# Kernel tuning notes

Measured on AMD Instinct MI355X. Metric: run time of the kernel, lower is better.

The kernel has to match this reference:

```python
import jax, jax.numpy as jnp
import numpy as np

DIM = 2048
HEADS = 16
HEAD_DIM = 128
B = 2
T = 2048


def _rope_as_in_source(x):
    # x: (b, h, t, d). FAITHFUL to the source bug: RotaryEmbedding uses
    # x.shape[1] (the HEADS axis, since it is called after transpose) as the
    # 'sequence' index, so rotation angle depends on head index and is
    # broadcast over the true sequence axis.
    n = x.shape[1]  # == heads
    d = x.shape[-1]
    inv_freq = 1.0 / (10000.0 ** (jnp.arange(0, d, 2, dtype=jnp.float32) / d))
    freqs = jnp.arange(n, dtype=jnp.float32)[:, None] * inv_freq[None, :]  # (h, d/2)
    cos = jnp.cos(freqs)[None, :, None, :]  # (1, h, 1, d/2)
    sin = jnp.sin(freqs)[None, :, None, :]
    x1 = x[..., 0::2]
    x2 = x[..., 1::2]
    out = jnp.stack([x1 * cos - x2 * sin, x1 * sin + x2 * cos], axis=-1)
    return out.reshape(x.shape)


def setup_inputs() -> dict:
    key = jax.random.key(0)
    ks = jax.random.split(key, 9)
    s_in = 1.0 / np.sqrt(DIM)
    hd = HEADS * HEAD_DIM
    s_o = 1.0 / np.sqrt(hd)
    return {
        "x": jax.random.normal(ks[0], (B, T, DIM), dtype=jnp.float32),
        "Wq": jax.random.normal(ks[1], (DIM, hd), dtype=jnp.float32) * s_in,
        "bq": jnp.zeros((hd,), dtype=jnp.float32),
        "Wk": jax.random.normal(ks[2], (DIM, hd), dtype=jnp.float32) * s_in,
        "bk": jnp.zeros((hd,), dtype=jnp.float32),
        "Wv": jax.random.normal(ks[3], (DIM, hd), dtype=jnp.float32) * s_in,
        "bv": jnp.zeros((hd,), dtype=jnp.float32),
        "Wo": jax.random.normal(ks[4], (hd, DIM), dtype=jnp.float32) * s_o,
        "bo": jnp.zeros((DIM,), dtype=jnp.float32),
    }


def reference(x, Wq, bq, Wk, bk, Wv, bv, Wo, bo):
    b, t, c = x.shape
    q = (x @ Wq + bq).reshape(b, t, HEADS, HEAD_DIM).transpose(0, 2, 1, 3)
    k = (x @ Wk + bk).reshape(b, t, HEADS, HEAD_DIM).transpose(0, 2, 1, 3)
    v = (x @ Wv + bv).reshape(b, t, HEADS, HEAD_DIM).transpose(0, 2, 1, 3)
    q = _rope_as_in_source(q)
    k = _rope_as_in_source(k)
    scale = 1.0 / np.sqrt(HEAD_DIM)
    scores = jnp.einsum("bhqd,bhkd->bhqk", q, k) * scale  # (b,h,t,t)
    attn = jax.nn.softmax(scores, axis=-1)
    out = jnp.einsum("bhqk,bhkd->bhqd", attn, v)  # (b,h,t,d)
    out = out.transpose(0, 2, 1, 3).reshape(b, t, HEADS * HEAD_DIM)
    return out @ Wo + bo
```

## Files before the change

kernel.cpp:

```cpp
#include <hip/hip_runtime.h>

typedef unsigned short ushort_t;
typedef unsigned int uint_t;
typedef __attribute__((ext_vector_type(8))) short short8;
typedef __attribute__((ext_vector_type(4))) float f32x4;
typedef __attribute__((ext_vector_type(4))) unsigned short ushort4_t;
typedef __attribute__((ext_vector_type(4))) unsigned int uint4_t;

__device__ inline ushort_t f2b(float f) {
    unsigned int x = __builtin_bit_cast(unsigned int, f);
    x += 0x7fffu + ((x >> 16) & 1u);
    return (ushort_t)(x >> 16);
}
__device__ inline uint_t cvt_pk_bf16(float lo, float hi) {
    uint_t r;
    asm("v_cvt_pk_bf16_f32 %0, %1, %2" : "=v"(r) : "v"(lo), "v"(hi));
    return r;
}

__device__ inline void gload16(const void* g, void* l) {
    __builtin_amdgcn_global_load_lds(
        (const __attribute__((address_space(1))) void*)g,
        (__attribute__((address_space(3))) void*)l, 16, 0, 0);
}

__global__ __launch_bounds__(256)
void cast_bf16(const float* __restrict__ src, ushort_t* __restrict__ dst) {
    size_t i = ((size_t)blockIdx.x * 256 + threadIdx.x) * 8;
    f32x4 a = *reinterpret_cast<const f32x4*>(src + i);
    f32x4 b = *reinterpret_cast<const f32x4*>(src + i + 4);
    short8 v;
#pragma unroll
    for (int j = 0; j < 4; ++j) { v[j] = (short)f2b(a[j]); v[4 + j] = (short)f2b(b[j]); }
    *reinterpret_cast<short8*>(dst + i) = v;
}

__global__ __launch_bounds__(64)
void transp4(const float* __restrict__ s0, const float* __restrict__ s1,
             const float* __restrict__ s2, const float* __restrict__ s3,
             ushort_t* __restrict__ d0, ushort_t* __restrict__ d1,
             ushort_t* __restrict__ d2, ushort_t* __restrict__ d3) {
    const int z = blockIdx.z;
    const float* src = (z == 0) ? s0 : (z == 1) ? s1 : (z == 2) ? s2 : s3;
    ushort_t* dst = (z == 0) ? d0 : (z == 1) ? d1 : (z == 2) ? d2 : d3;
    const int R = 2048, C = 2048;
    int r0 = blockIdx.x * 64 + ((threadIdx.x >> 3) << 3);
    int c0 = blockIdx.y * 64 + ((threadIdx.x & 7) << 3);
    ushort_t v[8][8];
#pragma unroll
    for (int i = 0; i < 8; ++i) {
        const float* p = src + (size_t)(r0 + i) * C + c0;
        f32x4 a = *reinterpret_cast<const f32x4*>(p);
        f32x4 b = *reinterpret_cast<const f32x4*>(p + 4);
#pragma unroll
        for (int j = 0; j < 4; ++j) { v[i][j] = f2b(a[j]); v[i][4 + j] = f2b(b[j]); }
    }
#pragma unroll
    for (int c = 0; c < 8; ++c) {
        short8 w;
#pragma unroll
        for (int i = 0; i < 8; ++i) w[i] = (short)v[i][c];
        *reinterpret_cast<short8*>(dst + (size_t)(c0 + c) * R + r0) = w;
    }
}

template <int MODE>
__global__ __launch_bounds__(256)
void gemm_qkv(const ushort_t* __restrict__ A, const ushort_t* __restrict__ Bt,
              const float* __restrict__ bias, ushort_t* __restrict__ C, float oscale) {
    const int K = 2048;
    __shared__ __align__(16) ushort_t As[128 * 64];
    __shared__ __align__(16) ushort_t Bs[128 * 64];
    const int tid = threadIdx.x, lane = tid & 63, wid = tid >> 6;
    const int l15 = lane & 15, g = lane >> 4;
    const int wr = wid >> 1, wc = wid & 1;
    const int m0 = blockIdx.y * 128, n0 = blockIdx.x * 128;
    f32x4 acc[4][4] = {};
    for (int k0 = 0; k0 < K; k0 += 64) {
#pragma unroll
        for (int is = 0; is < 4; ++is) {
            int c = is * 256 + tid;
            int row = c >> 3, sub = c & 7;
            int ks = (sub ^ (row & 7)) << 3;
            char* ldst = (char*)As + (size_t)(is * 256 + wid * 64) * 16;
            gload16(A + (size_t)(m0 + row) * K + k0 + ks, ldst);
            char* ldstB = (char*)Bs + (size_t)(is * 256 + wid * 64) * 16;
            gload16(Bt + (size_t)(n0 + row) * K + k0 + ks, ldstB);
        }
        __syncthreads();
#pragma unroll
        for (int kk = 0; kk < 2; ++kk) {
            short8 af[4], bf[4];
#pragma unroll
            for (int i = 0; i < 4; ++i) {
                int ra = wr * 64 + i * 16 + l15;
                af[i] = *reinterpret_cast<const short8*>(
                    (const char*)As + ra * 128 + (((4 * kk + g) ^ (ra & 7)) << 4));
                int rb = wc * 64 + i * 16 + l15;
                bf[i] = *reinterpret_cast<const short8*>(
                    (const char*)Bs + rb * 128 + (((4 * kk + g) ^ (rb & 7)) << 4));
            }
#pragma unroll
            for (int i = 0; i < 4; ++i)
#pragma unroll
                for (int j = 0; j < 4; ++j)
                    acc[i][j] = __builtin_amdgcn_mfma_f32_16x16x32_bf16(af[i], bf[j], acc[i][j], 0, 0, 0);
        }
        __syncthreads();
    }
#pragma unroll
    for (int j = 0; j < 4; ++j) {
        int n = n0 + wc * 64 + j * 16 + l15;
        float bj = bias[n];
        float sn = 0.f, cs = 1.f, sgn = 0.f;
        if (MODE == 0) {
            int d = n & 127, h = (n >> 7) & 15;
            float inv = expf(-(float)(d >> 1) * (9.210340371976184f / 64.0f));
            sincosf((float)h * inv, &sn, &cs);
            sgn = (d & 1) ? sn : -sn;
        }
#pragma unroll
        for (int i = 0; i < 4; ++i) {
            int mbase = m0 + wr * 64 + i * 16 + g * 4;
            if (MODE == 2) {
                int d = n & 127, hh = n >> 7;
                int b_ = mbase >> 11, t0 = mbase & 2047;
                ushort4_t w;
#pragma unroll
                for (int r = 0; r < 4; ++r) w[r] = f2b(acc[i][j][r] + bj);
                *reinterpret_cast<ushort4_t*>(
                    C + (((size_t)(b_ * 16 + hh) * 128 + d) * 2048 + t0)) = w;
            } else {
#pragma unroll
                for (int r = 0; r < 4; ++r) {
                    int m = mbase + r;
                    float v = acc[i][j][r] + bj;
                    float p = __shfl_xor(v, 1, 64);
                    v = fmaf(p, sgn, v * cs);
                    v *= oscale;
                    size_t addr = ((size_t)((m >> 11) * 16 + (n >> 7)) * 2048 + (m & 2047)) * 128 + (n & 127);
                    C[addr] = f2b(v);
                }
            }
        }
    }
}

__global__ __launch_bounds__(256)
void gemm_out(const ushort_t* __restrict__ A, const ushort_t* __restrict__ Bt,
              const float* __restrict__ bias, float* __restrict__ C,
              int M, int N, int K) {
    __shared__ __align__(16) ushort_t As[128 * 64];
    __shared__ __align__(16) ushort_t Bs[128 * 64];
    const int tid = threadIdx.x, lane = tid & 63, wid = tid >> 6;
    const int l15 = lane & 15, g = lane >> 4;
    const int wr = wid >> 1, wc = wid & 1;
    const int m0 = blockIdx.y * 128, n0 = blockIdx.x * 128;
    f32x4 acc[4][4] = {};
    for (int k0 = 0; k0 < K; k0 += 64) {
#pragma unroll
        for (int is = 0; is < 4; ++is) {
            int c = is * 256 + tid;
            int row = c >> 3, sub = c & 7;
            int ks = (sub ^ (row & 7)) << 3;
            char* ldst = (char*)As + (size_t)(is * 256 + wid * 64) * 16;
            gload16(A + (size_t)(m0 + row) * K + k0 + ks, ldst);
            char* ldstB = (char*)Bs + (size_t)(is * 256 + wid * 64) * 16;
            gload16(Bt + (size_t)(n0 + row) * K + k0 + ks, ldstB);
        }
        __syncthreads();
#pragma unroll
        for (int kk = 0; kk < 2; ++kk) {
            short8 af[4], bf[4];
#pragma unroll
            for (int i = 0; i < 4; ++i) {
                int ra = wr * 64 + i * 16 + l15;
                af[i] = *reinterpret_cast<const short8*>(
                    (const char*)As + ra * 128 + (((4 * kk + g) ^ (ra & 7)) << 4));
                int rb = wc * 64 + i * 16 + l15;
                bf[i] = *reinterpret_cast<const short8*>(
                    (const char*)Bs + rb * 128 + (((4 * kk + g) ^ (rb & 7)) << 4));
            }
#pragma unroll
            for (int i = 0; i < 4; ++i)
#pragma unroll
                for (int j = 0; j < 4; ++j)
                    acc[i][j] = __builtin_amdgcn_mfma_f32_16x16x32_bf16(af[i], bf[j], acc[i][j], 0, 0, 0);
        }
        __syncthreads();
    }
#pragma unroll
    for (int j = 0; j < 4; ++j) {
        int n = n0 + wc * 64 + j * 16 + l15;
        float bj = bias[n];
#pragma unroll
        for (int i = 0; i < 4; ++i) {
            int mbase = m0 + wr * 64 + i * 16 + g * 4;
#pragma unroll
            for (int r = 0; r < 4; ++r)
                C[(size_t)(mbase + r) * N + n] = acc[i][j][r] + bj;
        }
    }
}

__global__ __launch_bounds__(512)
void fattn(const ushort_t* __restrict__ Q, const ushort_t* __restrict__ K,
           const ushort_t* __restrict__ Vt, ushort_t* __restrict__ O) {
    __shared__ __align__(16) ushort_t Ks[2][64 * 128];
    __shared__ __align__(16) ushort_t Vs[2][128 * 64];
    const int tid = threadIdx.x, lane = tid & 63, wid = tid >> 6;
    const int l15 = lane & 15, g = lane >> 4;
    const int h = blockIdx.y, b = blockIdx.z;
    const size_t base = ((size_t)b * 16 + h) * (2048 * 128);
    const int q0 = blockIdx.x * 128 + wid * 16;
    const int q2 = l15 >> 2;
    const int sig = ((q2 == 1) ? 2 : (q2 == 2) ? 1 : q2) * 4 + (l15 & 3);
    short8 qf[4];
#pragma unroll
    for (int c = 0; c < 4; ++c)
        qf[c] = *reinterpret_cast<const short8*>(Q + base + (size_t)(q0 + l15) * 128 + c * 32 + g * 8);
    f32x4 oacc[8] = {};
    f32x4 oaccL = {};
    float m_r = -__builtin_inff();
    short8 ones;
#pragma unroll
    for (int j = 0; j < 8; ++j) ones[j] = (short)0x3F80;

    auto stage = [&](int kv0, int bsel) {
#pragma unroll
        for (int is = 0; is < 2; ++is) {
            {
                int c = is * 512 + tid;
                int row = c >> 4, sub = c & 15;
                int dsrc = (sub ^ (row & 7)) << 3;
                gload16(K + base + (size_t)(kv0 + row) * 128 + dsrc,
                        (char*)Ks[bsel] + (size_t)c * 16);
            }
            {
                int c = is * 512 + tid;
                int row = c >> 3, sub = c & 7;
                int tsrc = (sub ^ (row & 7)) << 3;
                gload16(Vt + base + (size_t)row * 2048 + kv0 + tsrc,
                        (char*)Vs[bsel] + (size_t)c * 16);
            }
        }
    };

    stage(0, 0);
    asm volatile("s_waitcnt vmcnt(0)" ::: "memory");
    __builtin_amdgcn_s_barrier();

    for (int it = 0; it < 32; ++it) {
        const int cur = it & 1;
        if (it < 31) stage((it + 1) << 6, cur ^ 1);
        f32x4 s[4] = {};
        __builtin_amdgcn_s_setprio(1);
#pragma unroll
        for (int nt = 0; nt < 4; ++nt) {
            int kvr = nt * 16 + sig;
#pragma unroll
            for (int c = 0; c < 4; ++c) {
                short8 kf = *reinterpret_cast<const short8*>(
                    (const char*)Ks[cur] + kvr * 256 + (((4 * c + g) ^ (sig & 7)) << 4));
                s[nt] = __builtin_amdgcn_mfma_f32_16x16x32_bf16(kf, qf[c], s[nt], 0, 0, 0);
            }
        }
        __builtin_amdgcn_s_setprio(0);
        float pm = fmaxf(fmaxf(fmaxf(s[0][0], s[0][1]), fmaxf(s[0][2], s[0][3])),
                         fmaxf(fmaxf(s[1][0], s[1][1]), fmaxf(s[1][2], s[1][3])));
        pm = fmaxf(pm, fmaxf(fmaxf(fmaxf(s[2][0], s[2][1]), fmaxf(s[2][2], s[2][3])),
                             fmaxf(fmaxf(s[3][0], s[3][1]), fmaxf(s[3][2], s[3][3]))));
        pm = fmaxf(pm, __shfl_xor(pm, 16, 64));
        pm = fmaxf(pm, __shfl_xor(pm, 32, 64));
        if (!__all(pm <= m_r + 5.0f)) {
            float mn = fmaxf(m_r, pm);
            float fac = exp2f(m_r - mn);
            m_r = mn;
#pragma unroll
            for (int r = 0; r < 4; ++r) oaccL[r] *= fac;
#pragma unroll
            for (int nt2 = 0; nt2 < 8; ++nt2)
#pragma unroll
                for (int r = 0; r < 4; ++r) oacc[nt2][r] *= fac;
        }
        uint_t W[4][2];
#pragma unroll
        for (int nt = 0; nt < 4; ++nt) {
            float p0 = exp2f(s[nt][0] - m_r);
            float p1 = exp2f(s[nt][1] - m_r);
            float p2 = exp2f(s[nt][2] - m_r);
            float p3 = exp2f(s[nt][3] - m_r);
            W[nt][0] = cvt_pk_bf16(p0, p1);
            W[nt][1] = cvt_pk_bf16(p2, p3);
        }
        __builtin_amdgcn_s_setprio(1);
#pragma unroll
        for (int ks = 0; ks < 2; ++ks) {
            uint_t A0 = W[2 * ks][0], A1 = W[2 * ks][1];
            uint_t B0 = W[2 * ks + 1][0], B1 = W[2 * ks + 1][1];
            asm("v_permlane32_swap_b32 %0, %1" : "+v"(A0), "+v"(B0));
            asm("v_permlane32_swap_b32 %0, %1" : "+v"(A1), "+v"(B1));
            uint4_t wv; wv[0] = A0; wv[1] = A1; wv[2] = B0; wv[3] = B1;
            short8 pb = __builtin_bit_cast(short8, wv);
            oaccL = __builtin_amdgcn_mfma_f32_16x16x32_bf16(ones, pb, oaccL, 0, 0, 0);
#pragma unroll
            for (int nt2 = 0; nt2 < 8; ++nt2) {
                int dr = nt2 * 16 + l15;
                short8 vb = *reinterpret_cast<const short8*>(
                    (const char*)Vs[cur] + dr * 128 + (((ks * 4 + g) ^ (dr & 7)) << 4));
                oacc[nt2] = __builtin_amdgcn_mfma_f32_16x16x32_bf16(vb, pb, oacc[nt2], 0, 0, 0);
            }
        }
        __builtin_amdgcn_s_setprio(0);
        asm volatile("s_waitcnt vmcnt(0)" ::: "memory");
        __builtin_amdgcn_s_barrier();
    }
    float inv = 1.f / oaccL[0];
    const size_t orow = ((size_t)b * 2048 + q0 + l15) * 2048 + (size_t)h * 128;
#pragma unroll
    for (int nt2 = 0; nt2 < 8; ++nt2) {
        ushort4_t w;
#pragma unroll
        for (int r = 0; r < 4; ++r) w[r] = f2b(oacc[nt2][r] * inv);
        *reinterpret_cast<ushort4_t*>(O + orow + nt2 * 16 + g * 4) = w;
    }
}

extern "C" void kernel_launch(void* const* d_in, const int* in_sizes, int n_in,
                              void* d_out, int out_size, void* d_ws, size_t ws_size,
                              hipStream_t stream) {
    const float* x  = (const float*)d_in[0];
    const float* Wq = (const float*)d_in[1];
    const float* bq = (const float*)d_in[2];
    const float* Wk = (const float*)d_in[3];
    const float* bk = (const float*)d_in[4];
    const float* Wv = (const float*)d_in[5];
    const float* bv = (const float*)d_in[6];
    const float* Wo = (const float*)d_in[7];
    const float* bo = (const float*)d_in[8];
    float* out = (float*)d_out;
    ushort_t* ws  = (ushort_t*)d_ws;

    const size_t WSZ = 2048ull * 2048;
    const size_t TSZ = 2ull * 16 * 2048 * 128;
    ushort_t* xb  = ws;
    ushort_t* Wtq = xb + TSZ;
    ushort_t* Wtk = Wtq + WSZ;
    ushort_t* Wtv = Wtk + WSZ;
    ushort_t* Wto = Wtv + WSZ;
    ushort_t* Qb  = Wto + WSZ;
    ushort_t* Kb  = Qb + TSZ;
    ushort_t* Vtb = Kb + TSZ;
    ushort_t* Sb  = Vtb + TSZ;

    const float QSC = 0.08838834764831845f * 1.4426950408889634f;

    cast_bf16<<<dim3(4096), 256, 0, stream>>>(x, xb);
    transp4<<<dim3(32, 32, 4), 64, 0, stream>>>(Wq, Wk, Wv, Wo, Wtq, Wtk, Wtv, Wto);

    gemm_qkv<0><<<dim3(16, 32), 256, 0, stream>>>(xb, Wtq, bq, Qb, QSC);
    gemm_qkv<0><<<dim3(16, 32), 256, 0, stream>>>(xb, Wtk, bk, Kb, 1.0f);
    gemm_qkv<2><<<dim3(16, 32), 256, 0, stream>>>(xb, Wtv, bv, Vtb, 1.0f);

    fattn<<<dim3(16, 16, 2), 512, 0, stream>>>(Qb, Kb, Vtb, Sb);

    gemm_out<<<dim3(16, 32), 256, 0, stream>>>(Sb, Wto, bo, out, 4096, 2048, 2048);
}
```

Measured before the change: 307.0 us.

## Switch flash attention to 32x32x16 MFMA tiles with 32 query rows per wave

Rewrites the attention kernel to use 32x32x16 bf16 MFMAs, so each wave handles 32 query rows instead of 16 and each block covers 256 queries. The grid is halved to match. Each K/V tile staged in LDS is therefore reused by twice as many queries, and fewer, larger MFMAs are issued. The row sum is now computed with VALU adds plus a cross-half shuffle instead of a ones-matrix MFMA. The trade-off is higher register pressure from 64 accumulator floats per lane, and fewer blocks (256) to fill the GPU.

```diff
diff --git a/kernel.cpp b/kernel.cpp
--- a/kernel.cpp
+++ b/kernel.cpp
@@ -4,6 +4,7 @@
 typedef unsigned int uint_t;
 typedef __attribute__((ext_vector_type(8))) short short8;
 typedef __attribute__((ext_vector_type(4))) float f32x4;
+typedef __attribute__((ext_vector_type(16))) float f32x16;
 typedef __attribute__((ext_vector_type(4))) unsigned short ushort4_t;
 typedef __attribute__((ext_vector_type(4))) unsigned int uint4_t;
 
@@ -203,28 +204,23 @@
     }
 }
 
-__global__ __launch_bounds__(512)
+__global__ __launch_bounds__(512, 4)
 void fattn(const ushort_t* __restrict__ Q, const ushort_t* __restrict__ K,
            const ushort_t* __restrict__ Vt, ushort_t* __restrict__ O) {
     __shared__ __align__(16) ushort_t Ks[2][64 * 128];
     __shared__ __align__(16) ushort_t Vs[2][128 * 64];
     const int tid = threadIdx.x, lane = tid & 63, wid = tid >> 6;
-    const int l15 = lane & 15, g = lane >> 4;
-    const int h = blockIdx.y, b = blockIdx.z;
-    const size_t base = ((size_t)b * 16 + h) * (2048 * 128);
-    const int q0 = blockIdx.x * 128 + wid * 16;
-    const int q2 = l15 >> 2;
-    const int sig = ((q2 == 1) ? 2 : (q2 == 2) ? 1 : q2) * 4 + (l15 & 3);
-    short8 qf[4];
-#pragma unroll
-    for (int c = 0; c < 4; ++c)
-        qf[c] = *reinterpret_cast<const short8*>(Q + base + (size_t)(q0 + l15) * 128 + c * 32 + g * 8);
-    f32x4 oacc[8] = {};
-    f32x4 oaccL = {};
-    float m_r = -__builtin_inff();
-    short8 ones;
-#pragma unroll
-    for (int j = 0; j < 8; ++j) ones[j] = (short)0x3F80;
+    const int l31 = lane & 31;
+    const int hl = (lane >> 5) & 1;
+    const int hd = blockIdx.y, b = blockIdx.z;
+    const size_t base = ((size_t)b * 16 + hd) * (2048 * 128);
+    const int q0 = blockIdx.x * 256 + wid * 32;
+    short8 qf[8];
+#pragma unroll
+    for (int kc = 0; kc < 8; ++kc)
+        qf[kc] = *reinterpret_cast<const short8*>(Q + base + (size_t)(q0 + l31) * 128 + kc * 16 + hl * 8);
+    f32x16 oacc[4] = {};
+    float m_r = -__builtin_inff(), l_r = 0.f;
 
     auto stage = [&](int kv0, int bsel) {
 #pragma unroll
@@ -253,76 +249,72 @@
     for (int it = 0; it < 32; ++it) {
         const int cur = it & 1;
         if (it < 31) stage((it + 1) << 6, cur ^ 1);
-        f32x4 s[4] = {};
-        __builtin_amdgcn_s_setprio(1);
-#pragma unroll
-        for (int nt = 0; nt < 4; ++nt) {
-            int kvr = nt * 16 + sig;
-#pragma unroll
-            for (int c = 0; c < 4; ++c) {
+#pragma unroll
+        for (int h = 0; h < 2; ++h) {
+            f32x16 s = {};
+            __builtin_amdgcn_s_setprio(1);
+#pragma unroll
+            for (int kc = 0; kc < 8; ++kc) {
                 short8 kf = *reinterpret_cast<const short8*>(
-                    (const char*)Ks[cur] + kvr * 256 + (((4 * c + g) ^ (sig & 7)) << 4));
-                s[nt] = __builtin_amdgcn_mfma_f32_16x16x32_bf16(kf, qf[c], s[nt], 0, 0, 0);
-            }
-        }
-        __builtin_amdgcn_s_setprio(0);
-        float pm = fmaxf(fmaxf(fmaxf(s[0][0], s[0][1]), fmaxf(s[0][2], s[0][3])),
-                         fmaxf(fmaxf(s[1][0], s[1][1]), fmaxf(s[1][2], s[1][3])));
-        pm = fmaxf(pm, fmaxf(fmaxf(fmaxf(s[2][0], s[2][1]), fmaxf(s[2][2], s[2][3])),
-                             fmaxf(fmaxf(s[3][0], s[3][1]), fmaxf(s[3][2], s[3][3]))));
-        pm = fmaxf(pm, __shfl_xor(pm, 16, 64));
-        pm = fmaxf(pm, __shfl_xor(pm, 32, 64));
-        if (!__all(pm <= m_r + 5.0f)) {
-            float mn = fmaxf(m_r, pm);
-            float fac = exp2f(m_r - mn);
-            m_r = mn;
-#pragma unroll
-            for (int r = 0; r < 4; ++r) oaccL[r] *= fac;
-#pragma unroll
-            for (int nt2 = 0; nt2 < 8; ++nt2)
-#pragma unroll
-                for (int r = 0; r < 4; ++r) oacc[nt2][r] *= fac;
-        }
-        uint_t W[4][2];
-#pragma unroll
-        for (int nt = 0; nt < 4; ++nt) {
-            float p0 = exp2f(s[nt][0] - m_r);
-            float p1 = exp2f(s[nt][1] - m_r);
-            float p2 = exp2f(s[nt][2] - m_r);
-            float p3 = exp2f(s[nt][3] - m_r);
-            W[nt][0] = cvt_pk_bf16(p0, p1);
-            W[nt][1] = cvt_pk_bf16(p2, p3);
-        }
-        __builtin_amdgcn_s_setprio(1);
-#pragma unroll
-        for (int ks = 0; ks < 2; ++ks) {
-            uint_t A0 = W[2 * ks][0], A1 = W[2 * ks][1];
-            uint_t B0 = W[2 * ks + 1][0], B1 = W[2 * ks + 1][1];
-            asm("v_permlane32_swap_b32 %0, %1" : "+v"(A0), "+v"(B0));
-            asm("v_permlane32_swap_b32 %0, %1" : "+v"(A1), "+v"(B1));
-            uint4_t wv; wv[0] = A0; wv[1] = A1; wv[2] = B0; wv[3] = B1;
-            short8 pb = __builtin_bit_cast(short8, wv);
-            oaccL = __builtin_amdgcn_mfma_f32_16x16x32_bf16(ones, pb, oaccL, 0, 0, 0);
-#pragma unroll
-            for (int nt2 = 0; nt2 < 8; ++nt2) {
-                int dr = nt2 * 16 + l15;
-                short8 vb = *reinterpret_cast<const short8*>(
-                    (const char*)Vs[cur] + dr * 128 + (((ks * 4 + g) ^ (dr & 7)) << 4));
-                oacc[nt2] = __builtin_amdgcn_mfma_f32_16x16x32_bf16(vb, pb, oacc[nt2], 0, 0, 0);
-            }
-        }
-        __builtin_amdgcn_s_setprio(0);
+                    (const char*)Ks[cur] + (h * 32 + l31) * 256 + (((2 * kc + hl) ^ (l31 & 7)) << 4));
+                s = __builtin_amdgcn_mfma_f32_32x32x16_bf16(kf, qf[kc], s, 0, 0, 0);
+            }
+            __builtin_amdgcn_s_setprio(0);
+            float pm = fmaxf(s[0], s[1]);
+#pragma unroll
+            for (int r = 2; r < 16; ++r) pm = fmaxf(pm, s[r]);
+            pm = fmaxf(pm, __shfl_xor(pm, 32, 64));
+            if (!__all(pm <= m_r + 5.0f)) {
+                float mn = fmaxf(m_r, pm);
+                float fac = exp2f(m_r - mn);
+                m_r = mn;
+                l_r *= fac;
+#pragma unroll
+                for (int dt = 0; dt < 4; ++dt)
+#pragma unroll
+                    for (int r = 0; r < 16; ++r) oacc[dt][r] *= fac;
+            }
+            float rs = 0.f;
+#pragma unroll
+            for (int r = 0; r < 16; ++r) { s[r] = exp2f(s[r] - m_r); rs += s[r]; }
+            rs += __shfl_xor(rs, 32, 64);
+            l_r += rs;
+            __builtin_amdgcn_s_setprio(1);
+#pragma unroll
+            for (int cc = 0; cc < 2; ++cc) {
+                uint_t X0 = cvt_pk_bf16(s[8 * cc + 0], s[8 * cc + 1]);
+                uint_t X1 = cvt_pk_bf16(s[8 * cc + 2], s[8 * cc + 3]);
+                uint_t Y0 = cvt_pk_bf16(s[8 * cc + 4], s[8 * cc + 5]);
+                uint_t Y1 = cvt_pk_bf16(s[8 * cc + 6], s[8 * cc + 7]);
+                asm("v_permlane32_swap_b32 %0, %1" : "+v"(X0), "+v"(Y0));
+                asm("v_permlane32_swap_b32 %0, %1" : "+v"(X1), "+v"(Y1));
+                uint4_t wv; wv[0] = X0; wv[1] = X1; wv[2] = Y0; wv[3] = Y1;
+                short8 pb = __builtin_bit_cast(short8, wv);
+                const int c = 2 * h + cc;
+#pragma unroll
+                for (int dt = 0; dt < 4; ++dt) {
+                    int dr = dt * 32 + l31;
+                    short8 vf = *reinterpret_cast<const short8*>(
+                        (const char*)Vs[cur] + dr * 128 + (((2 * c + hl) ^ (l31 & 7)) << 4));
+                    oacc[dt] = __builtin_amdgcn_mfma_f32_32x32x16_bf16(vf, pb, oacc[dt], 0, 0, 0);
+                }
+            }
+            __builtin_amdgcn_s_setprio(0);
+        }
         asm volatile("s_waitcnt vmcnt(0)" ::: "memory");
         __builtin_amdgcn_s_barrier();
     }
-    float inv = 1.f / oaccL[0];
-    const size_t orow = ((size_t)b * 2048 + q0 + l15) * 2048 + (size_t)h * 128;
-#pragma unroll
-    for (int nt2 = 0; nt2 < 8; ++nt2) {
-        ushort4_t w;
-#pragma unroll
-        for (int r = 0; r < 4; ++r) w[r] = f2b(oacc[nt2][r] * inv);
-        *reinterpret_cast<ushort4_t*>(O + orow + nt2 * 16 + g * 4) = w;
+    float inv = 1.f / l_r;
+    const size_t orow = ((size_t)b * 2048 + q0 + l31) * 2048 + (size_t)hd * 128;
+#pragma unroll
+    for (int dt = 0; dt < 4; ++dt) {
+#pragma unroll
+        for (int m = 0; m < 4; ++m) {
+            ushort4_t w;
+#pragma unroll
+            for (int i = 0; i < 4; ++i) w[i] = f2b(oacc[dt][4 * m + i] * inv);
+            *reinterpret_cast<ushort4_t*>(O + orow + dt * 32 + m * 8 + hl * 4) = w;
+        }
     }
 }
 
@@ -362,7 +354,7 @@
     gemm_qkv<0><<<dim3(16, 32), 256, 0, stream>>>(xb, Wtk, bk, Kb, 1.0f);
     gemm_qkv<2><<<dim3(16, 32), 256, 0, stream>>>(xb, Wtv, bv, Vtb, 1.0f);
 
-    fattn<<<dim3(16, 16, 2), 512, 0, stream>>>(Qb, Kb, Vtb, Sb);
+    fattn<<<dim3(8, 16, 2), 512, 0, stream>>>(Qb, Kb, Vtb, Sb);
 
     gemm_out<<<dim3(16, 32), 256, 0, stream>>>(Sb, Wto, bo, out, 4096, 2048, 2048);
 }
```

Result: slower. 373.6 us (+21.7%).

## Triple-buffer GEMM loads with 256x128 tiles and 512 threads, unify GEMM kernels

Applied to the files above, without the earlier changes.

The GEMM kernels are replaced by one templated kernel. It uses 512 threads, a 256x128 output tile per block, and a three-stage LDS ring of async global-to-LDS loads. Loads for tile t+2 are issued while tile t runs its MFMAs, with vmcnt waits and a single barrier per iteration in place of the two __syncthreads. MFMA sections are also raised in wave priority. The aim is to hide global load latency and cut barrier stalls, at the cost of much more LDS per block (144KB), which limits occupancy to one block per CU, and half as many blocks in the grid.

```diff
diff --git a/kernel.cpp b/kernel.cpp
--- a/kernel.cpp
+++ b/kernel.cpp
@@ -65,29 +65,44 @@
 }
 
 template <int MODE>
-__global__ __launch_bounds__(256)
-void gemm_qkv(const ushort_t* __restrict__ A, const ushort_t* __restrict__ Bt,
-              const float* __restrict__ bias, ushort_t* __restrict__ C, float oscale) {
+__global__ __launch_bounds__(512)
+void gemm_p(const ushort_t* __restrict__ A, const ushort_t* __restrict__ Bt,
+            const float* __restrict__ bias, void* __restrict__ Cv, float oscale) {
     const int K = 2048;
-    __shared__ __align__(16) ushort_t As[128 * 64];
-    __shared__ __align__(16) ushort_t Bs[128 * 64];
+    __shared__ __align__(16) ushort_t As[3][256 * 64];
+    __shared__ __align__(16) ushort_t Bs[3][128 * 64];
     const int tid = threadIdx.x, lane = tid & 63, wid = tid >> 6;
     const int l15 = lane & 15, g = lane >> 4;
     const int wr = wid >> 1, wc = wid & 1;
-    const int m0 = blockIdx.y * 128, n0 = blockIdx.x * 128;
-    f32x4 acc[4][4] = {};
-    for (int k0 = 0; k0 < K; k0 += 64) {
+    const int m0 = blockIdx.y * 256, n0 = blockIdx.x * 128;
+
+    auto stage = [&](int t, int buf) {
+        const int k0 = t << 6;
 #pragma unroll
         for (int is = 0; is < 4; ++is) {
-            int c = is * 256 + tid;
+            int c = is * 512 + tid;
             int row = c >> 3, sub = c & 7;
             int ks = (sub ^ (row & 7)) << 3;
-            char* ldst = (char*)As + (size_t)(is * 256 + wid * 64) * 16;
-            gload16(A + (size_t)(m0 + row) * K + k0 + ks, ldst);
-            char* ldstB = (char*)Bs + (size_t)(is * 256 + wid * 64) * 16;
-            gload16(Bt + (size_t)(n0 + row) * K + k0 + ks, ldstB);
-        }
-        __syncthreads();
+            gload16(A + (size_t)(m0 + row) * K + k0 + ks, (char*)As[buf] + (size_t)c * 16);
+        }
+#pragma unroll
+        for (int is = 0; is < 2; ++is) {
+            int c = is * 512 + tid;
+            int row = c >> 3, sub = c & 7;
+            int ks = (sub ^ (row & 7)) << 3;
+            gload16(Bt + (size_t)(n0 + row) * K + k0 + ks, (char*)Bs[buf] + (size_t)c * 16);
+        }
+    };
+
+    f32x4 acc[4][4] = {};
+    stage(0, 0);
+    stage(1, 1);
+    asm volatile("s_waitcnt vmcnt(6)" ::: "memory");
+    __builtin_amdgcn_s_barrier();
+
+    int buf = 0, bufn = 2;
+    for (int t = 0; t < 32; ++t) {
+        if (t < 30) stage(t + 2, bufn);
 #pragma unroll
         for (int kk = 0; kk < 2; ++kk) {
             short8 af[4], bf[4];
@@ -95,19 +110,26 @@
             for (int i = 0; i < 4; ++i) {
                 int ra = wr * 64 + i * 16 + l15;
                 af[i] = *reinterpret_cast<const short8*>(
-                    (const char*)As + ra * 128 + (((4 * kk + g) ^ (ra & 7)) << 4));
+                    (const char*)As[buf] + ra * 128 + (((4 * kk + g) ^ (ra & 7)) << 4));
                 int rb = wc * 64 + i * 16 + l15;
                 bf[i] = *reinterpret_cast<const short8*>(
-                    (const char*)Bs + rb * 128 + (((4 * kk + g) ^ (rb & 7)) << 4));
-            }
+                    (const char*)Bs[buf] + rb * 128 + (((4 * kk + g) ^ (rb & 7)) << 4));
+            }
+            __builtin_amdgcn_s_setprio(1);
 #pragma unroll
             for (int i = 0; i < 4; ++i)
 #pragma unroll
                 for (int j = 0; j < 4; ++j)
                     acc[i][j] = __builtin_amdgcn_mfma_f32_16x16x32_bf16(af[i], bf[j], acc[i][j], 0, 0, 0);
-        }
-        __syncthreads();
-    }
+            __builtin_amdgcn_s_setprio(0);
+        }
+        if (t < 30)       asm volatile("s_waitcnt vmcnt(6)" ::: "memory");
+        else if (t == 30) asm volatile("s_waitcnt vmcnt(0)" ::: "memory");
+        if (t < 31) __builtin_amdgcn_s_barrier();
+        buf = (buf == 2) ? 0 : buf + 1;
+        bufn = (bufn == 2) ? 0 : bufn + 1;
+    }
+
 #pragma unroll
     for (int j = 0; j < 4; ++j) {
         int n = n0 + wc * 64 + j * 16 + l15;
@@ -129,8 +151,8 @@
 #pragma unroll
                 for (int r = 0; r < 4; ++r) w[r] = f2b(acc[i][j][r] + bj);
                 *reinterpret_cast<ushort4_t*>(
-                    C + (((size_t)(b_ * 16 + hh) * 128 + d) * 2048 + t0)) = w;
-            } else {
+                    (ushort_t*)Cv + (((size_t)(b_ * 16 + hh) * 128 + d) * 2048 + t0)) = w;
+            } else if (MODE == 0) {
 #pragma unroll
                 for (int r = 0; r < 4; ++r) {
                     int m = mbase + r;
@@ -139,66 +161,13 @@
                     v = fmaf(p, sgn, v * cs);
                     v *= oscale;
                     size_t addr = ((size_t)((m >> 11) * 16 + (n >> 7)) * 2048 + (m & 2047)) * 128 + (n & 127);
-                    C[addr] = f2b(v);
+                    ((ushort_t*)Cv)[addr] = f2b(v);
                 }
-            }
-        }
-    }
-}
-
-__global__ __launch_bounds__(256)
-void gemm_out(const ushort_t* __restrict__ A, const ushort_t* __restrict__ Bt,
-              const float* __restrict__ bias, float* __restrict__ C,
-              int M, int N, int K) {
-    __shared__ __align__(16) ushort_t As[128 * 64];
-    __shared__ __align__(16) ushort_t Bs[128 * 64];
-    const int tid = threadIdx.x, lane = tid & 63, wid = tid >> 6;
-    const int l15 = lane & 15, g = lane >> 4;
-    const int wr = wid >> 1, wc = wid & 1;
-    const int m0 = blockIdx.y * 128, n0 = blockIdx.x * 128;
-    f32x4 acc[4][4] = {};
-    for (int k0 = 0; k0 < K; k0 += 64) {
-#pragma unroll
-        for (int is = 0; is < 4; ++is) {
-            int c = is * 256 + tid;
-            int row = c >> 3, sub = c & 7;
-            int ks = (sub ^ (row & 7)) << 3;
-            char* ldst = (char*)As + (size_t)(is * 256 + wid * 64) * 16;
-            gload16(A + (size_t)(m0 + row) * K + k0 + ks, ldst);
-            char* ldstB = (char*)Bs + (size_t)(is * 256 + wid * 64) * 16;
-            gload16(Bt + (size_t)(n0 + row) * K + k0 + ks, ldstB);
-        }
-        __syncthreads();
-#pragma unroll
-        for (int kk = 0; kk < 2; ++kk) {
-            short8 af[4], bf[4];
-#pragma unroll
-            for (int i = 0; i < 4; ++i) {
-                int ra = wr * 64 + i * 16 + l15;
-                af[i] = *reinterpret_cast<const short8*>(
-                    (const char*)As + ra * 128 + (((4 * kk + g) ^ (ra & 7)) << 4));
-                int rb = wc * 64 + i * 16 + l15;
-                bf[i] = *reinterpret_cast<const short8*>(
-                    (const char*)Bs + rb * 128 + (((4 * kk + g) ^ (rb & 7)) << 4));
-            }
-#pragma unroll
-            for (int i = 0; i < 4; ++i)
-#pragma unroll
-                for (int j = 0; j < 4; ++j)
-                    acc[i][j] = __builtin_amdgcn_mfma_f32_16x16x32_bf16(af[i], bf[j], acc[i][j], 0, 0, 0);
-        }
-        __syncthreads();
-    }
-#pragma unroll
-    for (int j = 0; j < 4; ++j) {
-        int n = n0 + wc * 64 + j * 16 + l15;
-        float bj = bias[n];
-#pragma unroll
-        for (int i = 0; i < 4; ++i) {
-            int mbase = m0 + wr * 64 + i * 16 + g * 4;
-#pragma unroll
-            for (int r = 0; r < 4; ++r)
-                C[(size_t)(mbase + r) * N + n] = acc[i][j][r] + bj;
+            } else {
+#pragma unroll
+                for (int r = 0; r < 4; ++r)
+                    ((float*)Cv)[(size_t)(mbase + r) * 2048 + n] = acc[i][j][r] + bj;
+            }
         }
     }
 }
@@ -358,11 +327,11 @@
     cast_bf16<<<dim3(4096), 256, 0, stream>>>(x, xb);
     transp4<<<dim3(32, 32, 4), 64, 0, stream>>>(Wq, Wk, Wv, Wo, Wtq, Wtk, Wtv, Wto);
 
-    gemm_qkv<0><<<dim3(16, 32), 256, 0, stream>>>(xb, Wtq, bq, Qb, QSC);
-    gemm_qkv<0><<<dim3(16, 32), 256, 0, stream>>>(xb, Wtk, bk, Kb, 1.0f);
-    gemm_qkv<2><<<dim3(16, 32), 256, 0, stream>>>(xb, Wtv, bv, Vtb, 1.0f);
+    gemm_p<0><<<dim3(16, 16), 512, 0, stream>>>(xb, Wtq, bq, Qb, QSC);
+    gemm_p<0><<<dim3(16, 16), 512, 0, stream>>>(xb, Wtk, bk, Kb, 1.0f);
+    gemm_p<2><<<dim3(16, 16), 512, 0, stream>>>(xb, Wtv, bv, Vtb, 1.0f);
 
     fattn<<<dim3(16, 16, 2), 512, 0, stream>>>(Qb, Kb, Vtb, Sb);
 
-    gemm_out<<<dim3(16, 32), 256, 0, stream>>>(Sb, Wto, bo, out, 4096, 2048, 2048);
-}
+    gemm_p<3><<<dim3(16, 16), 512, 0, stream>>>(Sb, Wto, bo, out, 1.0f);
+}
```

After: 322.6 us. +5.1%, slower.
